# Kernel optimization log

Measured on AMD Instinct MI355X. Metric: run time of the kernel, lower is better.

Reference implementation:

```python
import jax, jax.numpy as jnp
import numpy as np

ALPHA = 0.7
BETA = 0.3
GAMMA = 1.0
EPS = 1e-07


def setup_inputs() -> dict:
    key = jax.random.key(0)
    k1, k2 = jax.random.split(key)
    B, C, H, W = 8, 19, 512, 512
    inputs = jax.random.normal(k1, (B, C, H, W), dtype=jnp.float32)
    targets = jax.random.randint(k2, (B, H, W), 0, C, dtype=jnp.int64)
    return {"inputs": inputs, "targets": targets}


def reference(inputs, targets):
    # inputs: [B, C, H, W] logits; targets: [B, H, W] int labels
    B, C = inputs.shape[0], inputs.shape[1]
    probs = jax.nn.softmax(inputs, axis=1)  # [B, C, H, W]
    # one-hot target per class: [B, C, H, W]
    tgt = (targets[:, None, :, :] == jnp.arange(C)[None, :, None, None]).astype(probs.dtype)
    # per (b, c) reductions over spatial dims
    TP = jnp.sum(probs * tgt, axis=(2, 3))          # [B, C]
    FP = jnp.sum((1.0 - tgt) * probs, axis=(2, 3))  # [B, C]
    FN = jnp.sum(tgt * (1.0 - probs), axis=(2, 3))  # [B, C]
    tversky = (TP + EPS) / (TP + ALPHA * FN + BETA * FP + EPS)
    focal_tversky = (1.0 - tversky) ** GAMMA
    return jnp.sum(focal_tversky) / B
```

## Files before the change

### kernel.cpp

```cpp
#include <hip/hip_runtime.h>

#define NCLS 19
#define HWPIX (512 * 512)
#define NB 8
#define PB 64
#define ALPHA_C 0.7f
#define BETA_C 0.3f
#define EPS_C 1e-7f
#define L2E 1.44269504088896f

typedef float v2f __attribute__((ext_vector_type(2)));

__global__ __launch_bounds__(256, 3) void ftl_fused(
    const float* __restrict__ x,
    const int* __restrict__ tgt,
    float* __restrict__ part,
    int* __restrict__ counter,
    float* __restrict__ out) {
  const int b = blockIdx.x / PB;
  const int blk = blockIdx.x % PB;
  const int tid = threadIdx.x;

  __shared__ float sTPb[NCLS][32];
  __shared__ int sNb[NCLS][32];
  __shared__ float sS[NCLS];
  for (int i = tid; i < NCLS * 32; i += 256) {
    (&sTPb[0][0])[i] = 0.f;
    (&sNb[0][0])[i] = 0;
  }
  if (tid < NCLS) sS[tid] = 0.f;
  __syncthreads();

  const int quadsPerBlock = (HWPIX / 4) / PB;
  const int qbase = blk * quadsPerBlock;
  const float* xb = x + (size_t)b * NCLS * HWPIX;
  const int* tb = tgt + (size_t)b * HWPIX;
  const int cp = tid & 31;

  v2f S2[NCLS];
#pragma unroll
  for (int c = 0; c < NCLS; ++c) S2[c] = (v2f){0.f, 0.f};

  for (int q = tid; q < quadsPerBlock; q += 256) {
    const int pix = (qbase + q) * 4;
    const int4 t = *reinterpret_cast<const int4*>(tb + pix);

    v2f ea[NCLS], eb[NCLS];
    v2f sea = (v2f){0.f, 0.f}, seb = (v2f){0.f, 0.f};
#pragma unroll
    for (int c = 0; c < NCLS; ++c) {
      const float4 xv = *reinterpret_cast<const float4*>(xb + (size_t)c * HWPIX + pix);
      const v2f a = (v2f){xv.x, xv.y} * L2E;
      const v2f bb = (v2f){xv.z, xv.w} * L2E;
      ea[c] = (v2f){__builtin_amdgcn_exp2f(a.x), __builtin_amdgcn_exp2f(a.y)};
      eb[c] = (v2f){__builtin_amdgcn_exp2f(bb.x), __builtin_amdgcn_exp2f(bb.y)};
      sea += ea[c];
      seb += eb[c];
    }
    const v2f inva = (v2f){__builtin_amdgcn_rcpf(sea.x), __builtin_amdgcn_rcpf(sea.y)};
    const v2f invb = (v2f){__builtin_amdgcn_rcpf(seb.x), __builtin_amdgcn_rcpf(seb.y)};
#pragma unroll
    for (int c = 0; c < NCLS; ++c) {
      S2[c] += ea[c] * inva;
      S2[c] += eb[c] * invb;
    }

    const v2f xta = (v2f){xb[(size_t)t.x * HWPIX + pix + 0],
                          xb[(size_t)t.y * HWPIX + pix + 1]} * L2E;
    const v2f xtb = (v2f){xb[(size_t)t.z * HWPIX + pix + 2],
                          xb[(size_t)t.w * HWPIX + pix + 3]} * L2E;
    const v2f pta = (v2f){__builtin_amdgcn_exp2f(xta.x),
                          __builtin_amdgcn_exp2f(xta.y)} * inva;
    const v2f ptb = (v2f){__builtin_amdgcn_exp2f(xtb.x),
                          __builtin_amdgcn_exp2f(xtb.y)} * invb;
    atomicAdd(&sTPb[t.x][cp], pta.x);
    atomicAdd(&sTPb[t.y][cp], pta.y);
    atomicAdd(&sTPb[t.z][cp], ptb.x);
    atomicAdd(&sTPb[t.w][cp], ptb.y);
    atomicAdd(&sNb[t.x][cp], 1);
    atomicAdd(&sNb[t.y][cp], 1);
    atomicAdd(&sNb[t.z][cp], 1);
    atomicAdd(&sNb[t.w][cp], 1);
  }

#pragma unroll
  for (int c = 0; c < NCLS; ++c) {
    float Sc = S2[c].x + S2[c].y;
    for (int off = 32; off; off >>= 1) Sc += __shfl_down(Sc, off);
    if ((tid & 63) == 0) atomicAdd(&sS[c], Sc);
  }
  __syncthreads();
  if (tid < NCLS) {
    float tp = 0.f;
    int n = 0;
#pragma unroll
    for (int i = 0; i < 32; ++i) { tp += sTPb[tid][i]; n += sNb[tid][i]; }
    float* p = part + (size_t)blockIdx.x * (3 * NCLS);
    p[tid] = sS[tid];
    p[NCLS + tid] = tp;
    p[2 * NCLS + tid] = (float)n;
  }

  __syncthreads();
  __shared__ int lastFlag;
  if (tid == 0) {
    __threadfence();
    lastFlag = (atomicAdd(counter, 1) == (NB * PB - 1));
  }
  __syncthreads();
  if (!lastFlag) return;
  __threadfence();

  float v = 0.f;
  if (tid < NB * NCLS) {
    const int bb = tid / NCLS;
    const int c = tid % NCLS;
    float S = 0.f, TP = 0.f, Nc = 0.f;
#pragma unroll 16
    for (int p = 0; p < PB; ++p) {
      const float* q = part + (size_t)(bb * PB + p) * (3 * NCLS);
      S += q[c];
      TP += q[NCLS + c];
      Nc += q[2 * NCLS + c];
    }
    const float FPv = S - TP;
    const float FNv = Nc - TP;
    const float tv = (TP + EPS_C) / (TP + ALPHA_C * FNv + BETA_C * FPv + EPS_C);
    v = 1.0f - tv;
  }
  for (int off = 32; off; off >>= 1) v += __shfl_down(v, off);
  __shared__ float wsum[4];
  if ((tid & 63) == 0) wsum[tid >> 6] = v;
  __syncthreads();
  if (tid == 0) out[0] = (wsum[0] + wsum[1] + wsum[2] + wsum[3]) / (float)NB;
}

extern "C" void kernel_launch(void* const* d_in, const int* in_sizes, int n_in,
                              void* d_out, int out_size, void* d_ws, size_t ws_size,
                              hipStream_t stream) {
  const float* x = (const float*)d_in[0];
  const int* tgt = (const int*)d_in[1];
  float* out = (float*)d_out;
  float* part = (float*)d_ws;
  int* counter = (int*)(part + NB * PB * 3 * NCLS);

  hipMemsetAsync(counter, 0, sizeof(int), stream);
  ftl_fused<<<NB * PB, 256, 0, stream>>>(x, tgt, part, counter, out);
}
```

Measured before the change: 49.41 us.

## Recompute exp in second pass and accumulate TP in registers instead of LDS atomics

The kernel no longer keeps 38 exp values per thread in registers between the sum pass and the accumulate pass. It reloads the logits in a second pass (likely from cache) and recomputes the exponentials, which cuts register pressure. True-positive accumulation moves from per-pixel gather loads and LDS float atomics to per-class register accumulators using compare-select, followed by a wave reduction. The loop is hardcoded to 4 iterations, and an asm barrier stops the compiler from merging the two load streams. The cost is doubled exp work and doubled logit load traffic, which hits L2/L1 if the cache holds the lines.

Measured after the change: 83.78 us. 69.5% more time.

```diff
diff --git a/kernel.cpp b/kernel.cpp
--- a/kernel.cpp
+++ b/kernel.cpp
@@ -21,62 +21,58 @@
   const int blk = blockIdx.x % PB;
   const int tid = threadIdx.x;
 
-  __shared__ float sTPb[NCLS][32];
+  __shared__ float sS[NCLS], sTP[NCLS];
   __shared__ int sNb[NCLS][32];
-  __shared__ float sS[NCLS];
-  for (int i = tid; i < NCLS * 32; i += 256) {
-    (&sTPb[0][0])[i] = 0.f;
-    (&sNb[0][0])[i] = 0;
-  }
-  if (tid < NCLS) sS[tid] = 0.f;
+  for (int i = tid; i < NCLS * 32; i += 256) (&sNb[0][0])[i] = 0;
+  if (tid < NCLS) { sS[tid] = 0.f; sTP[tid] = 0.f; }
   __syncthreads();
 
-  const int quadsPerBlock = (HWPIX / 4) / PB;
-  const int qbase = blk * quadsPerBlock;
   const float* xb = x + (size_t)b * NCLS * HWPIX;
   const int* tb = tgt + (size_t)b * HWPIX;
   const int cp = tid & 31;
 
-  v2f S2[NCLS];
+  const float* xb2 = xb;
+  asm("" : "+s"(xb2));
+
+  v2f S2[NCLS], TP2[NCLS];
 #pragma unroll
-  for (int c = 0; c < NCLS; ++c) S2[c] = (v2f){0.f, 0.f};
+  for (int c = 0; c < NCLS; ++c) {
+    S2[c] = (v2f){0.f, 0.f};
+    TP2[c] = (v2f){0.f, 0.f};
+  }
 
-  for (int q = tid; q < quadsPerBlock; q += 256) {
-    const int pix = (qbase + q) * 4;
+  const int base = blk * 4096;
+  for (int it = 0; it < 4; ++it) {
+    const int pix = base + it * 1024 + tid * 4;
     const int4 t = *reinterpret_cast<const int4*>(tb + pix);
 
-    v2f ea[NCLS], eb[NCLS];
-    v2f sea = (v2f){0.f, 0.f}, seb = (v2f){0.f, 0.f};
+    v2f sa = (v2f){0.f, 0.f}, sb = (v2f){0.f, 0.f};
 #pragma unroll
     for (int c = 0; c < NCLS; ++c) {
-      const float4 xv = *reinterpret_cast<const float4*>(xb + (size_t)c * HWPIX + pix);
-      const v2f a = (v2f){xv.x, xv.y} * L2E;
-      const v2f bb = (v2f){xv.z, xv.w} * L2E;
-      ea[c] = (v2f){__builtin_amdgcn_exp2f(a.x), __builtin_amdgcn_exp2f(a.y)};
-      eb[c] = (v2f){__builtin_amdgcn_exp2f(bb.x), __builtin_amdgcn_exp2f(bb.y)};
-      sea += ea[c];
-      seb += eb[c];
+      const float4 xv =
+          *reinterpret_cast<const float4*>(xb + (size_t)c * HWPIX + pix);
+      sa += (v2f){__builtin_amdgcn_exp2f(xv.x * L2E),
+                  __builtin_amdgcn_exp2f(xv.y * L2E)};
+      sb += (v2f){__builtin_amdgcn_exp2f(xv.z * L2E),
+                  __builtin_amdgcn_exp2f(xv.w * L2E)};
     }
-    const v2f inva = (v2f){__builtin_amdgcn_rcpf(sea.x), __builtin_amdgcn_rcpf(sea.y)};
-    const v2f invb = (v2f){__builtin_amdgcn_rcpf(seb.x), __builtin_amdgcn_rcpf(seb.y)};
+    const v2f inva = (v2f){__builtin_amdgcn_rcpf(sa.x),
+                           __builtin_amdgcn_rcpf(sa.y)};
+    const v2f invb = (v2f){__builtin_amdgcn_rcpf(sb.x),
+                           __builtin_amdgcn_rcpf(sb.y)};
+
 #pragma unroll
     for (int c = 0; c < NCLS; ++c) {
-      S2[c] += ea[c] * inva;
-      S2[c] += eb[c] * invb;
+      const float4 xv =
+          *reinterpret_cast<const float4*>(xb2 + (size_t)c * HWPIX + pix);
+      const v2f pa = (v2f){__builtin_amdgcn_exp2f(xv.x * L2E),
+                           __builtin_amdgcn_exp2f(xv.y * L2E)} * inva;
+      const v2f pb = (v2f){__builtin_amdgcn_exp2f(xv.z * L2E),
+                           __builtin_amdgcn_exp2f(xv.w * L2E)} * invb;
+      S2[c] += pa + pb;
+      TP2[c] += (v2f){(t.x == c ? pa.x : 0.f) + (t.z == c ? pb.x : 0.f),
+                      (t.y == c ? pa.y : 0.f) + (t.w == c ? pb.y : 0.f)};
     }
-
-    const v2f xta = (v2f){xb[(size_t)t.x * HWPIX + pix + 0],
-                          xb[(size_t)t.y * HWPIX + pix + 1]} * L2E;
-    const v2f xtb = (v2f){xb[(size_t)t.z * HWPIX + pix + 2],
-                          xb[(size_t)t.w * HWPIX + pix + 3]} * L2E;
-    const v2f pta = (v2f){__builtin_amdgcn_exp2f(xta.x),
-                          __builtin_amdgcn_exp2f(xta.y)} * inva;
-    const v2f ptb = (v2f){__builtin_amdgcn_exp2f(xtb.x),
-                          __builtin_amdgcn_exp2f(xtb.y)} * invb;
-    atomicAdd(&sTPb[t.x][cp], pta.x);
-    atomicAdd(&sTPb[t.y][cp], pta.y);
-    atomicAdd(&sTPb[t.z][cp], ptb.x);
-    atomicAdd(&sTPb[t.w][cp], ptb.y);
     atomicAdd(&sNb[t.x][cp], 1);
     atomicAdd(&sNb[t.y][cp], 1);
     atomicAdd(&sNb[t.z][cp], 1);
@@ -86,18 +82,24 @@
 #pragma unroll
   for (int c = 0; c < NCLS; ++c) {
     float Sc = S2[c].x + S2[c].y;
-    for (int off = 32; off; off >>= 1) Sc += __shfl_down(Sc, off);
-    if ((tid & 63) == 0) atomicAdd(&sS[c], Sc);
+    float Tc = TP2[c].x + TP2[c].y;
+    for (int off = 32; off; off >>= 1) {
+      Sc += __shfl_down(Sc, off);
+      Tc += __shfl_down(Tc, off);
+    }
+    if ((tid & 63) == 0) {
+      atomicAdd(&sS[c], Sc);
+      atomicAdd(&sTP[c], Tc);
+    }
   }
   __syncthreads();
   if (tid < NCLS) {
-    float tp = 0.f;
     int n = 0;
 #pragma unroll
-    for (int i = 0; i < 32; ++i) { tp += sTPb[tid][i]; n += sNb[tid][i]; }
+    for (int i = 0; i < 32; ++i) n += sNb[tid][i];
     float* p = part + (size_t)blockIdx.x * (3 * NCLS);
     p[tid] = sS[tid];
-    p[NCLS + tid] = tp;
+    p[NCLS + tid] = sTP[tid];
     p[2 * NCLS + tid] = (float)n;
   }
 
```
